# Performance work log

Hardware: AMD Instinct MI355X
Metric: run time of the kernel (lower is better)

The kernel has to match this reference:

```python
import jax, jax.numpy as jnp
import numpy as np

B, T, D, H = 2, 2048, 1024, 16
DK = D // H
NEG = -1e9  # stand-in for -inf; causal mask guarantees >=1 valid key per row


def setup_inputs() -> dict:
    key = jax.random.key(0)
    ks = jax.random.split(key, 9)
    s = 1.0 / np.sqrt(D)
    x = jax.random.normal(ks[0], (B, T, D), dtype=jnp.float32)
    mask = jnp.broadcast_to(jnp.tril(jnp.ones((T, T), dtype=jnp.int32))[None, None], (B, 1, T, T))
    params = {}
    for i, n in enumerate(['q', 'k', 'v', 'o']):
        params['W' + n] = jax.random.normal(ks[1 + 2 * i], (D, D), dtype=jnp.float32) * s
        params['b' + n] = jax.random.normal(ks[2 + 2 * i], (D,), dtype=jnp.float32) * s
    return dict(x=x, mask=mask, **params)


def reference(x, mask, Wq, bq, Wk, bk, Wv, bv, Wo, bo):
    Bx, Tx, Dx = x.shape
    # projections: [B,T,D] -> [B,H,T,DK]
    def split_heads(y):
        return y.reshape(Bx, Tx, H, DK).transpose(0, 2, 1, 3)
    Q = split_heads(x @ Wq + bq)
    K = split_heads(x @ Wk + bk)
    V = split_heads(x @ Wv + bv)
    scores = jnp.einsum('bhqd,bhkd->bhqk', Q, K) / jnp.sqrt(jnp.float32(DK))
    scores = jnp.where(mask == 0, NEG, scores)
    attn = jax.nn.softmax(scores, axis=-1)  # dropout is identity in eval / p=0
    out = jnp.einsum('bhqk,bhkd->bhqd', attn, V)
    out = out.transpose(0, 2, 1, 3).reshape(Bx, Tx, Dx)
    return out @ Wo + bo
```

## Files before the change

### kernel.cpp

```cpp
#include <hip/hip_runtime.h>
#include <hip/hip_bf16.h>

typedef __bf16 bf16;
typedef __attribute__((ext_vector_type(8))) __bf16 bf16x8;
typedef __attribute__((ext_vector_type(4))) __bf16 bf16x4;
typedef __attribute__((ext_vector_type(4))) float f32x4;

#define TSEQ 2048
#define DMODEL 1024
#define NHEAD 16
#define DKH 64
#define BATCH 2
#define NQKV 3072
#define PSTR 72

typedef __attribute__((address_space(1))) const void gv_t;
typedef __attribute__((address_space(3))) void sv_t;
__device__ __forceinline__ void gll16(const bf16* g, bf16* s) {
    __builtin_amdgcn_global_load_lds((gv_t*)g, (sv_t*)s, 16, 0, 0);
}
__device__ __forceinline__ void wait_vm0() {
    __builtin_amdgcn_s_waitcnt(0x0F70);
}

__global__ __launch_bounds__(256) void convert_bf16(
    const float* __restrict__ in, bf16* __restrict__ out)
{
    int i = (blockIdx.x * 256 + threadIdx.x) * 4;
    f32x4 v = *(const f32x4*)(in + i);
    bf16x4 o;
#pragma unroll
    for (int j = 0; j < 4; ++j) o[j] = (bf16)v[j];
    *(bf16x4*)(out + i) = o;
}

__global__ __launch_bounds__(256) void bias_concat(
    const float* __restrict__ bq, const float* __restrict__ bk,
    const float* __restrict__ bv, float* __restrict__ out)
{
    int i = blockIdx.x * 256 + threadIdx.x;
    float v = i < 1024 ? bq[i] : i < 2048 ? bk[i - 1024] : bv[i - 2048];
    out[i] = v;
}

__global__ __launch_bounds__(256) void transpose_w(
    const float* __restrict__ W0, const float* __restrict__ W1,
    const float* __restrict__ W2, const float* __restrict__ W3,
    bf16* __restrict__ WT)
{
    __shared__ float t[32][33];
    const float* W = blockIdx.z == 0 ? W0 : blockIdx.z == 1 ? W1
                   : blockIdx.z == 2 ? W2 : W3;
    bf16* T = WT + (size_t)blockIdx.z * DMODEL * DMODEL;
    int bx = blockIdx.x * 32, by = blockIdx.y * 32;
    int tx = threadIdx.x, ty = threadIdx.y;
#pragma unroll
    for (int i = 0; i < 4; ++i)
        t[ty + i * 8][tx] = W[(size_t)(by + ty + i * 8) * DMODEL + bx + tx];
    __syncthreads();
#pragma unroll
    for (int i = 0; i < 4; ++i)
        T[(size_t)(bx + ty + i * 8) * DMODEL + by + tx] = (bf16)t[tx][ty + i * 8];
}

__global__ __launch_bounds__(256) void transpose_v(
    const bf16* __restrict__ QKV, bf16* __restrict__ VT)
{
    __shared__ bf16 t[32][33];
    int b = blockIdx.z >> 4, h = blockIdx.z & 15;
    int t0 = blockIdx.x * 32, d0 = blockIdx.y * 32;
    int tx = threadIdx.x, ty = threadIdx.y;
#pragma unroll
    for (int i = 0; i < 4; ++i)
        t[ty + i * 8][tx] =
            QKV[(size_t)(b * TSEQ + t0 + ty + i * 8) * NQKV + 2048 + h * DKH + d0 + tx];
    __syncthreads();
#pragma unroll
    for (int i = 0; i < 4; ++i)
        VT[((size_t)(b * NHEAD + h) * DKH + d0 + ty + i * 8) * TSEQ + t0 + tx] =
            t[tx][ty + i * 8];
}

template <typename OutT>
__global__ __launch_bounds__(256) void gemm_bias_kernel(
    const bf16* __restrict__ A, const bf16* __restrict__ BT,
    const float* __restrict__ bias, OutT* __restrict__ C, int ldc)
{
    __shared__ bf16 As[128 * 32];
    __shared__ bf16 Bs[128 * 32];
    const int tid = threadIdx.x;
    const int ln = tid & 63, wave = tid >> 6;
    const int wm = wave >> 1, wn = wave & 1;
    const int lr = ln & 15, quad = ln >> 4;
    const int m0 = blockIdx.y * 128, n0 = blockIdx.x * 128;

    f32x4 acc[4][4] = {};

    const int grow = wave * 32 + (ln >> 2);
    const int gcol = (ln & 3) * 8;
    const bf16* Ag = A + (size_t)(m0 + grow) * DMODEL + gcol;
    const bf16* Bg = BT + (size_t)(n0 + grow) * DMODEL + gcol;
    bf16* AsW = As + wave * 1024;
    bf16* BsW = Bs + wave * 1024;

    for (int kt = 0; kt < DMODEL / 32; ++kt) {
        const int kk = kt * 32;
#pragma unroll
        for (int l = 0; l < 2; ++l) {
            gll16(Ag + (size_t)(l * 16) * DMODEL + kk, AsW + l * 512);
            gll16(Bg + (size_t)(l * 16) * DMODEL + kk, BsW + l * 512);
        }
        wait_vm0();
        __syncthreads();
        bf16x8 af[4], bfr[4];
#pragma unroll
        for (int i = 0; i < 4; ++i)
            af[i] = *(const bf16x8*)(As + (wm * 64 + i * 16 + lr) * 32 + quad * 8);
#pragma unroll
        for (int j = 0; j < 4; ++j)
            bfr[j] = *(const bf16x8*)(Bs + (wn * 64 + j * 16 + lr) * 32 + quad * 8);
#pragma unroll
        for (int i = 0; i < 4; ++i)
#pragma unroll
            for (int j = 0; j < 4; ++j)
                acc[i][j] = __builtin_amdgcn_mfma_f32_16x16x32_bf16(
                    af[i], bfr[j], acc[i][j], 0, 0, 0);
        __syncthreads();
    }

#pragma unroll
    for (int j = 0; j < 4; ++j) {
        int n = n0 + wn * 64 + j * 16 + lr;
        float bv = bias[n];
#pragma unroll
        for (int i = 0; i < 4; ++i) {
            int mb = m0 + wm * 64 + i * 16 + quad * 4;
#pragma unroll
            for (int r = 0; r < 4; ++r)
                C[(size_t)(mb + r) * ldc + n] = (OutT)(acc[i][j][r] + bv);
        }
    }
}

template <bool MASK>
__device__ __forceinline__ void attn_chunk(
    int kc, int q0w, int lr, int quad,
    const bf16* __restrict__ KsB, const bf16* __restrict__ VsB,
    bf16* __restrict__ Pw,
    const bf16x8 qb[2], f32x4 oacc[4], float& lrow)
{
    const int sw = lr & 7;
    bf16x8 kb[4][2];
#pragma unroll
    for (int kt = 0; kt < 4; ++kt)
#pragma unroll
        for (int kk = 0; kk < 2; ++kk)
            kb[kt][kk] = *(const bf16x8*)(KsB + (kt * 16 + lr) * 64 +
                                          (((kk * 4 + quad) ^ sw) * 8));
    f32x4 st[4] = {};
#pragma unroll
    for (int kt = 0; kt < 4; ++kt)
#pragma unroll
        for (int kk = 0; kk < 2; ++kk)
            st[kt] = __builtin_amdgcn_mfma_f32_16x16x32_bf16(
                kb[kt][kk], qb[kk], st[kt], 0, 0, 0);

    const float scale2 = 0.18033688f;
    const int q = q0w + lr;
    float rs = 0.f;
#pragma unroll
    for (int kt = 0; kt < 4; ++kt) {
        bf16x4 p4;
#pragma unroll
        for (int r = 0; r < 4; ++r) {
            float p = exp2f(fmaf(st[kt][r], scale2, -24.0f));
            if (MASK && (kc + kt * 16 + quad * 4 + r > q)) p = 0.f;
            rs += p;
            p4[r] = (bf16)p;
        }
        *(bf16x4*)(Pw + lr * PSTR + kt * 16 + quad * 4) = p4;
    }
    rs += __shfl_xor(rs, 16);
    rs += __shfl_xor(rs, 32);
    lrow += rs;

#pragma unroll
    for (int kk = 0; kk < 2; ++kk) {
        bf16x8 pa = *(const bf16x8*)(Pw + lr * PSTR + kk * 32 + quad * 8);
#pragma unroll
        for (int dt = 0; dt < 4; ++dt) {
            bf16x8 vb = *(const bf16x8*)(VsB + (dt * 16 + lr) * 64 +
                                         (((kk * 4 + quad) ^ sw) * 8));
            oacc[dt] = __builtin_amdgcn_mfma_f32_16x16x32_bf16(
                pa, vb, oacc[dt], 0, 0, 0);
        }
    }
}

__global__ __launch_bounds__(512) void flash_attn(
    const bf16* __restrict__ QKV, const bf16* __restrict__ VT,
    bf16* __restrict__ O)
{
    __shared__ bf16 Ks[2][64 * 64];
    __shared__ bf16 Vs[2][64 * 64];
    __shared__ bf16 Pl[8][16 * PSTR];
    const int tid = threadIdx.x;
    const int ln = tid & 63, w = tid >> 6;
    const int lr = ln & 15, quad = ln >> 4;
    const int h = blockIdx.y, b = blockIdx.z;

    int xb = blockIdx.x;
    if ((h ^ b) & 1) xb = (TSEQ / 128 - 1) - xb;
    const int q0 = xb * 128;
    const int q0w = q0 + w * 16;
    bf16* Pw = Pl[w];

    const bf16* Qb = QKV + (size_t)b * TSEQ * NQKV + h * DKH;
    const bf16* Kb = Qb + 1024;
    const bf16* VTb = VT + (size_t)(b * NHEAD + h) * DKH * TSEQ;

    const int srow = (w & 3) * 16 + (ln >> 3);
    const int scol = ((ln & 7) ^ ((ln >> 3) & 7)) * 8;
    const bool stK = (w < 4);

    auto stage = [&](int buf, int kc) {
        if (stK) {
            const bf16* g = Kb + (size_t)(kc + srow) * NQKV + scol;
            bf16* s = &Ks[buf][(w & 3) * 16 * 64];
#pragma unroll
            for (int l = 0; l < 2; ++l)
                gll16(g + (size_t)(l * 8) * NQKV, s + l * 8 * 64);
        } else {
            const bf16* g = VTb + (size_t)srow * TSEQ + kc + scol;
            bf16* s = &Vs[buf][(w & 3) * 16 * 64];
#pragma unroll
            for (int l = 0; l < 2; ++l)
                gll16(g + (size_t)(l * 8) * TSEQ, s + l * 8 * 64);
        }
    };

    bf16x8 qb[2];
#pragma unroll
    for (int kk = 0; kk < 2; ++kk)
        qb[kk] = *(const bf16x8*)(Qb + (size_t)(q0w + lr) * NQKV +
                                  kk * 32 + quad * 8);

    f32x4 oacc[4] = {};
    float lrow = 0.f;

    const int nch = (q0 + 128) >> 6;
    stage(0, 0);
    wait_vm0();
    __syncthreads();
    for (int c = 0; c < nch; ++c) {
        if (c + 1 < nch) stage((c + 1) & 1, (c + 1) * 64);
        const int kc = c * 64;
        if (kc <= q0w + 15) {
            if (kc + 63 <= q0w)
                attn_chunk<false>(kc, q0w, lr, quad, Ks[c & 1], Vs[c & 1], Pw,
                                  qb, oacc, lrow);
            else
                attn_chunk<true>(kc, q0w, lr, quad, Ks[c & 1], Vs[c & 1], Pw,
                                 qb, oacc, lrow);
        }
        wait_vm0();
        __syncthreads();
    }

#pragma unroll
    for (int r = 0; r < 4; ++r) {
        float inv = 1.0f / __shfl(lrow, quad * 4 + r);
        int row = q0w + quad * 4 + r;
#pragma unroll
        for (int dt = 0; dt < 4; ++dt)
            O[(size_t)(b * TSEQ + row) * DMODEL + h * DKH + dt * 16 + lr] =
                (bf16)(oacc[dt][r] * inv);
    }
}

extern "C" void kernel_launch(void* const* d_in, const int* in_sizes, int n_in,
                              void* d_out, int out_size, void* d_ws, size_t ws_size,
                              hipStream_t stream)
{
    const float* x  = (const float*)d_in[0];
    const float* Wq = (const float*)d_in[2];
    const float* bq = (const float*)d_in[3];
    const float* Wk = (const float*)d_in[4];
    const float* bk = (const float*)d_in[5];
    const float* Wv = (const float*)d_in[6];
    const float* bv = (const float*)d_in[7];
    const float* Wo = (const float*)d_in[8];
    const float* bo = (const float*)d_in[9];

    char* ws = (char*)d_ws;
    bf16* xb   = (bf16*)(ws);
    bf16* QKV  = (bf16*)(ws + (8u  << 20));
    bf16* VT   = (bf16*)(ws + (32u << 20));
    bf16* O    = (bf16*)(ws + (40u << 20));
    bf16* WT   = (bf16*)(ws + (48u << 20));
    float* wsBias = (float*)VT;

    const int NX = BATCH * TSEQ * DMODEL;
    convert_bf16<<<NX / (256 * 4), 256, 0, stream>>>(x, xb);

    dim3 tb(32, 8);
    transpose_w<<<dim3(32, 32, 4), tb, 0, stream>>>(Wq, Wk, Wv, Wo, WT);
    bias_concat<<<NQKV / 256, 256, 0, stream>>>(bq, bk, bv, wsBias);

    gemm_bias_kernel<bf16><<<dim3(NQKV / 128, 32), 256, 0, stream>>>(
        xb, WT, wsBias, QKV, NQKV);

    transpose_v<<<dim3(TSEQ / 32, DKH / 32, BATCH * NHEAD), tb, 0, stream>>>(QKV, VT);

    flash_attn<<<dim3(TSEQ / 128, NHEAD, BATCH), 512, 0, stream>>>(QKV, VT, O);

    gemm_bias_kernel<float><<<dim3(DMODEL / 128, 32), 256, 0, stream>>>(
        O, WT + 3u * (1u << 20), bo, (float*)d_out, DMODEL);
}
```

Measured before the change: 217.5 us.

## Fuse V transpose into QKV GEMM epilogue, double-buffer GEMM, smaller output tiles

```diff
diff --git a/kernel.cpp b/kernel.cpp
--- a/kernel.cpp
+++ b/kernel.cpp
@@ -63,81 +63,96 @@
         T[(size_t)(bx + ty + i * 8) * DMODEL + by + tx] = (bf16)t[tx][ty + i * 8];
 }
 
-__global__ __launch_bounds__(256) void transpose_v(
-    const bf16* __restrict__ QKV, bf16* __restrict__ VT)
-{
-    __shared__ bf16 t[32][33];
-    int b = blockIdx.z >> 4, h = blockIdx.z & 15;
-    int t0 = blockIdx.x * 32, d0 = blockIdx.y * 32;
-    int tx = threadIdx.x, ty = threadIdx.y;
-#pragma unroll
-    for (int i = 0; i < 4; ++i)
-        t[ty + i * 8][tx] =
-            QKV[(size_t)(b * TSEQ + t0 + ty + i * 8) * NQKV + 2048 + h * DKH + d0 + tx];
-    __syncthreads();
-#pragma unroll
-    for (int i = 0; i < 4; ++i)
-        VT[((size_t)(b * NHEAD + h) * DKH + d0 + ty + i * 8) * TSEQ + t0 + tx] =
-            t[tx][ty + i * 8];
-}
-
-template <typename OutT>
+template <int MT, typename OutT>
 __global__ __launch_bounds__(256) void gemm_bias_kernel(
     const bf16* __restrict__ A, const bf16* __restrict__ BT,
-    const float* __restrict__ bias, OutT* __restrict__ C, int ldc)
-{
-    __shared__ bf16 As[128 * 32];
-    __shared__ bf16 Bs[128 * 32];
+    const float* __restrict__ bias, OutT* __restrict__ C, int ldc,
+    bf16* __restrict__ Vout)
+{
+    constexpr int BM = MT * 32;
+    constexpr int AISS = BM / 64;
+    __shared__ bf16 As[2][BM * 32];
+    __shared__ bf16 Bs[2][128 * 32];
     const int tid = threadIdx.x;
     const int ln = tid & 63, wave = tid >> 6;
     const int wm = wave >> 1, wn = wave & 1;
     const int lr = ln & 15, quad = ln >> 4;
-    const int m0 = blockIdx.y * 128, n0 = blockIdx.x * 128;
-
-    f32x4 acc[4][4] = {};
-
-    const int grow = wave * 32 + (ln >> 2);
+    const int m0 = blockIdx.y * BM, n0 = blockIdx.x * 128;
+
+    f32x4 acc[MT][4] = {};
+
+    const int arow = wave * 16 * AISS + (ln >> 2);
+    const int brow = wave * 32 + (ln >> 2);
     const int gcol = (ln & 3) * 8;
-    const bf16* Ag = A + (size_t)(m0 + grow) * DMODEL + gcol;
-    const bf16* Bg = BT + (size_t)(n0 + grow) * DMODEL + gcol;
-    bf16* AsW = As + wave * 1024;
-    bf16* BsW = Bs + wave * 1024;
+    const bf16* Ag = A + (size_t)(m0 + arow) * DMODEL + gcol;
+    const bf16* Bg = BT + (size_t)(n0 + brow) * DMODEL + gcol;
+
+    auto stage = [&](int buf, int kk) {
+#pragma unroll
+        for (int l = 0; l < AISS; ++l)
+            gll16(Ag + (size_t)(l * 16) * DMODEL + kk,
+                  As[buf] + wave * 512 * AISS + l * 512);
+#pragma unroll
+        for (int l = 0; l < 2; ++l)
+            gll16(Bg + (size_t)(l * 16) * DMODEL + kk,
+                  Bs[buf] + wave * 1024 + l * 512);
+    };
+
+    stage(0, 0);
+    wait_vm0();
+    __syncthreads();
 
     for (int kt = 0; kt < DMODEL / 32; ++kt) {
-        const int kk = kt * 32;
-#pragma unroll
-        for (int l = 0; l < 2; ++l) {
-            gll16(Ag + (size_t)(l * 16) * DMODEL + kk, AsW + l * 512);
-            gll16(Bg + (size_t)(l * 16) * DMODEL + kk, BsW + l * 512);
-        }
-        wait_vm0();
-        __syncthreads();
-        bf16x8 af[4], bfr[4];
-#pragma unroll
-        for (int i = 0; i < 4; ++i)
-            af[i] = *(const bf16x8*)(As + (wm * 64 + i * 16 + lr) * 32 + quad * 8);
+        if (kt + 1 < DMODEL / 32) stage((kt + 1) & 1, (kt + 1) * 32);
+        const bf16* Asb = As[kt & 1];
+        const bf16* Bsb = Bs[kt & 1];
+        bf16x8 af[MT], bfr[4];
+#pragma unroll
+        for (int i = 0; i < MT; ++i)
+            af[i] = *(const bf16x8*)(Asb + (wm * (BM / 2) + i * 16 + lr) * 32 + quad * 8);
 #pragma unroll
         for (int j = 0; j < 4; ++j)
-            bfr[j] = *(const bf16x8*)(Bs + (wn * 64 + j * 16 + lr) * 32 + quad * 8);
-#pragma unroll
-        for (int i = 0; i < 4; ++i)
+            bfr[j] = *(const bf16x8*)(Bsb + (wn * 64 + j * 16 + lr) * 32 + quad * 8);
+#pragma unroll
+        for (int i = 0; i < MT; ++i)
 #pragma unroll
             for (int j = 0; j < 4; ++j)
                 acc[i][j] = __builtin_amdgcn_mfma_f32_16x16x32_bf16(
                     af[i], bfr[j], acc[i][j], 0, 0, 0);
+        wait_vm0();
         __syncthreads();
     }
 
-#pragma unroll
-    for (int j = 0; j < 4; ++j) {
-        int n = n0 + wn * 64 + j * 16 + lr;
-        float bv = bias[n];
-#pragma unroll
-        for (int i = 0; i < 4; ++i) {
-            int mb = m0 + wm * 64 + i * 16 + quad * 4;
-#pragma unroll
-            for (int r = 0; r < 4; ++r)
-                C[(size_t)(mb + r) * ldc + n] = (OutT)(acc[i][j][r] + bv);
+    if (MT == 4 && Vout != nullptr && n0 >= 2048) {
+        const int bb = m0 >> 11;
+        const int tb_ = (m0 & (TSEQ - 1)) + wm * 64;
+#pragma unroll
+        for (int j = 0; j < 4; ++j) {
+            int n = n0 + wn * 64 + j * 16 + lr;
+            int hd = n - 2048;
+            float bv = bias[n];
+            bf16* vrow = Vout + ((size_t)(bb * DMODEL + hd)) * TSEQ;
+#pragma unroll
+            for (int i = 0; i < MT; ++i) {
+                int t = tb_ + i * 16 + quad * 4;
+                bf16x4 v4;
+#pragma unroll
+                for (int r = 0; r < 4; ++r) v4[r] = (bf16)(acc[i][j][r] + bv);
+                *(bf16x4*)(vrow + t) = v4;
+            }
+        }
+    } else {
+#pragma unroll
+        for (int j = 0; j < 4; ++j) {
+            int n = n0 + wn * 64 + j * 16 + lr;
+            float bv = bias[n];
+#pragma unroll
+            for (int i = 0; i < MT; ++i) {
+                int mb = m0 + wm * (BM / 2) + i * 16 + quad * 4;
+#pragma unroll
+                for (int r = 0; r < 4; ++r)
+                    C[(size_t)(mb + r) * ldc + n] = (OutT)(acc[i][j][r] + bv);
+            }
         }
     }
 }
@@ -298,7 +313,7 @@
     bf16* VT   = (bf16*)(ws + (32u << 20));
     bf16* O    = (bf16*)(ws + (40u << 20));
     bf16* WT   = (bf16*)(ws + (48u << 20));
-    float* wsBias = (float*)VT;
+    float* wsBias = (float*)O;
 
     const int NX = BATCH * TSEQ * DMODEL;
     convert_bf16<<<NX / (256 * 4), 256, 0, stream>>>(x, xb);
@@ -307,13 +322,11 @@
     transpose_w<<<dim3(32, 32, 4), tb, 0, stream>>>(Wq, Wk, Wv, Wo, WT);
     bias_concat<<<NQKV / 256, 256, 0, stream>>>(bq, bk, bv, wsBias);
 
-    gemm_bias_kernel<bf16><<<dim3(NQKV / 128, 32), 256, 0, stream>>>(
-        xb, WT, wsBias, QKV, NQKV);
-
-    transpose_v<<<dim3(TSEQ / 32, DKH / 32, BATCH * NHEAD), tb, 0, stream>>>(QKV, VT);
+    gemm_bias_kernel<4, bf16><<<dim3(NQKV / 128, 32), 256, 0, stream>>>(
+        xb, WT, wsBias, QKV, NQKV, VT);
 
     flash_attn<<<dim3(TSEQ / 128, NHEAD, BATCH), 512, 0, stream>>>(QKV, VT, O);
 
-    gemm_bias_kernel<float><<<dim3(DMODEL / 128, 32), 256, 0, stream>>>(
-        O, WT + 3u * (1u << 20), bo, (float*)d_out, DMODEL);
-}
+    gemm_bias_kernel<2, float><<<dim3(DMODEL / 128, 64), 256, 0, stream>>>(
+        O, WT + 3u * (1u << 20), bo, (float*)d_out, DMODEL, nullptr);
+}
```

Measured after the change: 230.4 us. 5.9% more time.
